# Kernel optimization log

Measured on AMD Instinct MI355X. Metric: run time of the kernel, lower is better.

## Reference

```python
import jax, jax.numpy as jnp
import numpy as np
from jax import lax

B = 256
R_ITERS = 3

def squash(x):
    # x * |x| / (1 + |x|^2), applied along last axis
    n = jnp.linalg.norm(x, axis=-1, keepdims=True)
    return x * n / (1.0 + n * n)

def conv2d(x, w, b, stride):
    y = lax.conv_general_dilated(x, w, window_strides=(stride, stride), padding='VALID',
                                 dimension_numbers=('NCHW', 'OIHW', 'NCHW'))
    return y + b[None, :, None, None]

def setup_inputs() -> dict:
    key = jax.random.key(0)
    ks = jax.random.split(key, 12)
    s = 0.05
    return {
        'x': jax.random.normal(ks[0], (B, 1, 28, 28), jnp.float32),
        'label': jax.random.randint(ks[1], (B,), 0, 10),
        'conv1_w': jax.random.normal(ks[2], (256, 1, 9, 9), jnp.float32) * s,
        'conv1_b': jnp.zeros((256,), jnp.float32),
        'pconv_w': jax.random.normal(ks[3], (256, 256, 9, 9), jnp.float32) * s,
        'pconv_b': jnp.zeros((256,), jnp.float32),
        'W_dig': jax.random.normal(ks[4], (1152, 10, 16, 8), jnp.float32),
        'dec_w1': jax.random.normal(ks[5], (512, 160), jnp.float32) * s,
        'dec_b1': jnp.zeros((512,), jnp.float32),
        'dec_w2': jax.random.normal(ks[6], (1024, 512), jnp.float32) * s,
        'dec_b2': jnp.zeros((1024,), jnp.float32),
        'dec_w3': jax.random.normal(ks[7], (784, 1024), jnp.float32) * s,
        'dec_b3': jnp.zeros((784,), jnp.float32),
    }

def reference(x, label, conv1_w, conv1_b, pconv_w, pconv_b, W_dig,
              dec_w1, dec_b1, dec_w2, dec_b2, dec_w3, dec_b3):
    # conv stem: [B,1,28,28] -> [B,256,20,20]
    h = conv2d(x, conv1_w, conv1_b, 1)
    # primary caps conv: -> [B,256,6,6] -> [B,1152,8] -> squash
    h = conv2d(h, pconv_w, pconv_b, 2)
    caps = squash(h.reshape(h.shape[0], -1, 8))
    # prediction vectors u_hat: [B, 1152, 10, 16]
    u = jnp.einsum('iond,bid->bion', W_dig, caps)
    # dynamic routing (softmax over input-capsule axis, per original code)
    b = jnp.zeros_like(u)
    for r in range(1, R_ITERS + 1):
        c = jax.nn.softmax(b, axis=1)
        s = (c * u).sum(axis=1, keepdims=True)     # [B,1,10,16]
        v = squash(s)
        if r != R_ITERS:
            b = b + (v * u).sum(axis=-1, keepdims=True)
    v = v.squeeze(1)                               # [B,10,16]
    # masked reconstruction
    one_hot = jax.nn.one_hot(label, 10, dtype=v.dtype)
    recon = (one_hot[..., None] * v).reshape(v.shape[0], 160)
    recon = jax.nn.relu(recon @ dec_w1.T + dec_b1)
    recon = jax.nn.relu(recon @ dec_w2.T + dec_b2)
    recon = jax.nn.sigmoid(recon @ dec_w3.T + dec_b3)
    return (v, recon, one_hot)
```

## Files before the change

### kernel.cpp

```cpp
#include <hip/hip_runtime.h>
#include <hip/hip_bf16.h>
#include <stdint.h>


typedef short short8 __attribute__((ext_vector_type(8)));
typedef unsigned short u16x8 __attribute__((ext_vector_type(8)));
typedef float f32x4  __attribute__((ext_vector_type(4)));

__device__ inline float bf2f(unsigned short u) {
    unsigned int v = ((unsigned int)u) << 16;
    float f;
    __builtin_memcpy(&f, &v, 4);
    return f;
}
__device__ inline unsigned short f2bf(float f) {
    __hip_bfloat16 h = __float2bfloat16(f);
    unsigned short u;
    __builtin_memcpy(&u, &h, 2);
    return u;
}
__device__ inline float clampf(float x, float b) {
    return fminf(fmaxf(x, -b), b);
}
__device__ inline float rdf(const void* p, size_t i, int f) {
    return f ? ((const float*)p)[i] : bf2f(((const unsigned short*)p)[i]);
}
__device__ inline void gload_lds16(const unsigned short* g, unsigned short* l) {
    __builtin_amdgcn_global_load_lds(
        (const __attribute__((address_space(1))) void*)g,
        (__attribute__((address_space(3))) void*)l, 16, 0, 0);
}
__device__ inline int detect_f(const void* w1c) {
    const unsigned short* w = (const unsigned short*)w1c;
    int lane = threadIdx.x & 63;
    int cnt = 0;
#pragma unroll
    for (int j = 0; j < 4; ++j) {
        float v = fabsf(bf2f(w[lane * 4 + j]));
        if (v > 100.f) cnt++;
    }
#pragma unroll
    for (int off = 32; off; off >>= 1) cnt += __shfl_xor(cnt, off);
    return cnt >= 4;
}

__global__ __launch_bounds__(256) void k_prep(
        const void* __restrict__ w1c, const void* __restrict__ w2c,
        float* __restrict__ h2f, unsigned short* __restrict__ B1p,
        unsigned short* __restrict__ Bp3) {
    __shared__ unsigned short wl[20736];
    int blk = blockIdx.x, tid = threadIdx.x;
    if (blk < 2304) {
        ((f32x4*)h2f)[blk * 256 + tid] = (f32x4){0.f, 0.f, 0.f, 0.f};
    } else if (blk < 2400) {
        int f = detect_f(w1c);
        int idx = (blk - 2304) * 256 + tid;
        int co = idx / 96, k = idx - co * 96;
        B1p[idx] = (k < 81) ? f2bf(rdf(w1c, (size_t)co * 81 + k, f)) : (unsigned short)0;
    } else {
        int f = detect_f(w1c);
        int co = blk - 2400;
        size_t base = (size_t)co * 20736;
        for (int i = tid; i < 20736; i += 256)
            wl[i] = f2bf(rdf(w2c, base + i, f));
        __syncthreads();
        for (int idx = tid; idx < 20736; idx += 256) {
            int t = idx >> 8, ci = idx & 255;
            int kc = ci >> 6, cin = ci & 63;
            Bp3[((size_t)(t * 4 + kc) << 14) + (co << 6) + cin] = wl[ci * 81 + t];
        }
    }
}

__global__ __launch_bounds__(256) void k_prep2(
        const void* __restrict__ wdig, const void* __restrict__ dw2,
        const void* __restrict__ dw3, const void* __restrict__ w1c,
        unsigned short* __restrict__ Wdb2,
        unsigned short* __restrict__ w2b,
        unsigned short* __restrict__ w3b) {
    __shared__ unsigned short wl[20480];
    int f = detect_f(w1c);
    int blk = blockIdx.x, tid = threadIdx.x;
    if (blk < 72) {
        int i0 = blk * 16;
        size_t base = (size_t)i0 * 1280;
        for (int idx = tid; idx < 20480; idx += 256)
            wl[idx] = f2bf(rdf(wdig, base + idx, f));
        __syncthreads();
        if (tid < 160) {
            int o = tid / 16, n = tid - o * 16;
            unsigned short* dst = Wdb2 + (size_t)o * 147456 + n * 9216 + i0 * 8;
            const unsigned short* src = wl + tid * 8;
#pragma unroll
            for (int i = 0; i < 16; ++i)
                *(uint4*)(dst + i * 8) = *(const uint4*)(src + i * 1280);
        }
    } else if (blk < 2120) {
        int idx = (blk - 72) * 256 + tid;
        w2b[idx] = f2bf(rdf(dw2, idx, f));
    } else {
        int idx = (blk - 2120) * 256 + tid;
        w3b[idx] = (idx < 802816) ? f2bf(rdf(dw3, idx, f)) : (unsigned short)0;
    }
}

__global__ __launch_bounds__(256) void k_conv1(
        const void* __restrict__ x,
        const unsigned short* __restrict__ B1p,
        const void* __restrict__ bias,
        unsigned short* __restrict__ h1p,
        const void* __restrict__ w1c) {
    __shared__ unsigned short xl[1568];
    __shared__ int offt[96];
    int f = detect_f(w1c);
    int tid = threadIdx.x;
    if (tid < 96) offt[tid] = (tid < 81) ? (tid / 9) * 28 + (tid % 9) : 0;

    int mblk = blockIdx.x * 128;
    int bfirst = mblk / 400;
    int blast = (mblk + 127) / 400;
    int nload = (blast - bfirst + 1) * 784;
    for (int i = tid; i < nload; i += 256)
        xl[i] = f2bf(rdf(x, (size_t)bfirst * 784 + i, f));
    __syncthreads();

    int wave = tid >> 6, lane = tid & 63;
    int wr = wave >> 1, wc = wave & 1;
    int mbase = mblk + wr * 64;
    int nbase = blockIdx.y * 128 + wc * 64;
    int l15 = lane & 15, l4 = lane >> 4;

    int lbase[4];
#pragma unroll
    for (int mt = 0; mt < 4; ++mt) {
        int m = mbase + mt * 16 + l15;
        int img = m / 400 - bfirst, pos = m % 400;
        lbase[mt] = img * 784 + (pos / 20) * 28 + (pos % 20);
    }

    f32x4 acc[4][4];
#pragma unroll
    for (int mt = 0; mt < 4; ++mt)
#pragma unroll
        for (int nt = 0; nt < 4; ++nt)
            acc[mt][nt] = (f32x4){0.f, 0.f, 0.f, 0.f};

#pragma unroll
    for (int kc = 0; kc < 3; ++kc) {
        int kbase = kc * 32 + l4 * 8;
        short8 af[4], bfr[4];
#pragma unroll
        for (int mt = 0; mt < 4; ++mt)
#pragma unroll
            for (int j = 0; j < 8; ++j) {
                int k = kbase + j;
                af[mt][j] = (k < 81) ? (short)xl[lbase[mt] + offt[k]] : (short)0;
            }
#pragma unroll
        for (int nt = 0; nt < 4; ++nt)
            bfr[nt] = *(const short8*)(B1p + (size_t)(nbase + nt * 16 + l15) * 96 + kbase);
#pragma unroll
        for (int mt = 0; mt < 4; ++mt)
#pragma unroll
            for (int nt = 0; nt < 4; ++nt)
                acc[mt][nt] = __builtin_amdgcn_mfma_f32_16x16x32_bf16(
                    af[mt], bfr[nt], acc[mt][nt], 0, 0, 0);
    }

#pragma unroll
    for (int mt = 0; mt < 4; ++mt)
#pragma unroll
        for (int nt = 0; nt < 4; ++nt) {
            int col = nbase + nt * 16 + l15;
            float bv = rdf(bias, col, f);
#pragma unroll
            for (int r = 0; r < 4; ++r) {
                int row = mbase + mt * 16 + l4 * 4 + r;
                h1p[(size_t)row * 256 + col] = f2bf(clampf(acc[mt][nt][r] + bv, 1024.f));
            }
        }
}

__global__ __launch_bounds__(256) void k_conv2(
        const unsigned short* __restrict__ h1p,
        const unsigned short* __restrict__ Bp,
        float* __restrict__ h2f) {
    __shared__ unsigned short As[2][4096];
    __shared__ unsigned short Bs[2][4096];
    int tid = threadIdx.x;
    int wave = tid >> 6, lane = tid & 63;
    int wr = wave >> 1, wc = wave & 1;
    int mb = blockIdx.x * 128, nb = blockIdx.y * 128;
    int s = blockIdx.z;
    int t0 = (81 * s) >> 3, t1 = (81 * (s + 1)) >> 3;
    int l15 = lane & 15, l4 = lane >> 4;

    int rsub = lane >> 2;
    int slog = (lane & 3) ^ ((lane >> 3) & 3);
    int aoff[2], boff[2];
#pragma unroll
    for (int r = 0; r < 2; ++r) {
        int row = wave * 32 + r * 16 + rsub;
        int m = mb + row;
        int bb = m / 36, pos = m - bb * 36;
        int y = pos / 6, xx = pos - y * 6;
        aoff[r] = (bb * 400 + y * 40 + xx * 2) * 256 + slog * 8;
        boff[r] = row * 64 + slog * 8;
    }

    int ko = (l4 ^ ((l15 >> 1) & 3)) << 3;
    int arow[4], brow[4];
#pragma unroll
    for (int mt = 0; mt < 4; ++mt) arow[mt] = ((wr * 64 + mt * 16 + l15) << 5) + ko;
#pragma unroll
    for (int nt = 0; nt < 4; ++nt) brow[nt] = ((wc * 64 + nt * 16 + l15) << 5) + ko;

    f32x4 acc[4][4];
#pragma unroll
    for (int mt = 0; mt < 4; ++mt)
#pragma unroll
        for (int nt = 0; nt < 4; ++nt)
            acc[mt][nt] = (f32x4){0.f, 0.f, 0.f, 0.f};

    int skc = 0;
    int sky = t0 / 9, skx = t0 - sky * 9;
    int stadd = (sky * 20 + skx) << 8;
    int st4 = t0 * 4;

    auto stage = [&](int buf) {
        const unsigned short* aw = h1p + stadd + (skc << 5);
        const unsigned short* bw = Bp + (((size_t)(st4 + (skc >> 1))) << 14)
                                     + nb * 64 + ((skc & 1) << 5);
        unsigned short* al = &As[buf][wave << 10];
        unsigned short* bl = &Bs[buf][wave << 10];
#pragma unroll
        for (int r = 0; r < 2; ++r) {
            gload_lds16(aw + aoff[r], al + (r << 9));
            gload_lds16(bw + boff[r], bl + (r << 9));
        }
    };
    auto adv = [&]() {
        if (++skc == 8) {
            skc = 0; st4 += 4;
            if (++skx == 9) { skx = 0; stadd += 3072; }
            else            { stadd += 256; }
        }
    };
    auto compute = [&](int buf) {
        short8 af[4], bfr[4];
#pragma unroll
        for (int mt = 0; mt < 4; ++mt)
            af[mt] = *(const short8*)(&As[buf][arow[mt]]);
#pragma unroll
        for (int nt = 0; nt < 4; ++nt)
            bfr[nt] = *(const short8*)(&Bs[buf][brow[nt]]);
#pragma unroll
        for (int mt = 0; mt < 4; ++mt)
#pragma unroll
            for (int nt = 0; nt < 4; ++nt)
                acc[mt][nt] = __builtin_amdgcn_mfma_f32_16x16x32_bf16(
                    af[mt], bfr[nt], acc[mt][nt], 0, 0, 0);
    };

    int nit = (t1 - t0) * 8;
    stage(0); adv();
    asm volatile("s_waitcnt vmcnt(0)" ::: "memory");
    __builtin_amdgcn_s_barrier();
    int cur = 0;
    for (int i = 0; i < nit; ++i) {
        if (i + 1 < nit) { stage(cur ^ 1); adv(); }
        compute(cur);
        asm volatile("s_waitcnt vmcnt(0)" ::: "memory");
        __builtin_amdgcn_s_barrier();
        cur ^= 1;
    }

#pragma unroll
    for (int mt = 0; mt < 4; ++mt)
#pragma unroll
        for (int nt = 0; nt < 4; ++nt) {
            int col = nb + wc * 64 + nt * 16 + l15;
#pragma unroll
            for (int r = 0; r < 4; ++r) {
                int row = mb + wr * 64 + mt * 16 + l4 * 4 + r;
                atomicAdd(&h2f[(size_t)row * 256 + col], acc[mt][nt][r]);
            }
        }
}

__global__ __launch_bounds__(256) void k_caps2(
        const float* __restrict__ h2f, const void* __restrict__ pb,
        unsigned short* __restrict__ caps, const void* __restrict__ w1c) {
    __shared__ float ld[9216];
    int f = detect_f(w1c);
    int b = blockIdx.x, tid = threadIdx.x;
#pragma unroll 4
    for (int p = 0; p < 36; ++p)
        ld[p * 256 + tid] = h2f[(size_t)b * 9216 + p * 256 + tid];
    __syncthreads();
    for (int c = tid; c < 1152; c += 256) {
        float h[8], ss = 0.f;
#pragma unroll
        for (int d = 0; d < 8; ++d) {
            int flat = c * 8 + d;
            int co = flat / 36, pos = flat - co * 36;
            float v = clampf(ld[pos * 256 + co] + rdf(pb, co, f), 20000.f);
            h[d] = v;
            ss += v * v;
        }
        float sc = sqrtf(ss) / (1.f + ss);
        u16x8 cv;
#pragma unroll
        for (int d = 0; d < 8; ++d) cv[d] = f2bf(h[d] * sc);
        *(u16x8*)(caps + ((size_t)b * 1152 + c) * 8) = cv;
    }
}

__global__ __launch_bounds__(384) void k_routing(
        const unsigned short* __restrict__ caps, const unsigned short* __restrict__ Wdb2,
        const int* __restrict__ label, void* __restrict__ d_out,
        float* __restrict__ vsel, const void* __restrict__ w1c) {
    int f = detect_f(w1c);
    int bo = blockIdx.x;
    int b = bo / 10, o = bo - b * 10;
    int tid = threadIdx.x;
    int wid = tid >> 6, lane = tid & 63;

    __shared__ float redw[6][16];
    __shared__ float sbuf[16];
    __shared__ float mred[8];
    __shared__ float sred[8];

    float u[3][16];
    float a[3] = {0.f, 0.f, 0.f};
    const unsigned short* capb = caps + (size_t)b * 9216;
    const unsigned short* wob = Wdb2 + (size_t)o * 147456;

#pragma unroll
    for (int r = 0; r < 3; ++r) {
        int i = tid + r * 384;
        u16x8 cq = *(const u16x8*)(capb + i * 8);
        float cf[8];
#pragma unroll
        for (int d = 0; d < 8; ++d) cf[d] = bf2f(cq[d]);
#pragma unroll
        for (int n = 0; n < 16; ++n) {
            u16x8 q = *(const u16x8*)(wob + ((size_t)n * 1152 + i) * 8);
            float sacc = 0.f;
#pragma unroll
            for (int d = 0; d < 8; ++d) sacc += bf2f(q[d]) * cf[d];
            u[r][n] = sacc;
        }
    }

    for (int rr = 1; rr <= 3; ++rr) {
        float mx = fmaxf(fmaxf(a[0], a[1]), a[2]);
#pragma unroll
        for (int off = 32; off; off >>= 1) mx = fmaxf(mx, __shfl_xor(mx, off));
        if (lane == 0) mred[wid] = mx;
        __syncthreads();
        float M = mred[0];
#pragma unroll
        for (int w = 1; w < 6; ++w) M = fmaxf(M, mred[w]);

        float e[3], es = 0.f;
#pragma unroll
        for (int r = 0; r < 3; ++r) { e[r] = __expf(a[r] - M); es += e[r]; }
#pragma unroll
        for (int off = 32; off; off >>= 1) es += __shfl_xor(es, off);
        if (lane == 0) sred[wid] = es;
        __syncthreads();
        float S = 0.f;
#pragma unroll
        for (int w = 0; w < 6; ++w) S += sred[w];
        float inv = 1.f / S;

        float p[16];
#pragma unroll
        for (int n = 0; n < 16; ++n)
            p[n] = (e[0] * u[0][n] + e[1] * u[1][n] + e[2] * u[2][n]) * inv;
#pragma unroll
        for (int n = 0; n < 16; ++n)
#pragma unroll
            for (int off = 32; off; off >>= 1) p[n] += __shfl_xor(p[n], off);
        if (lane == 0)
#pragma unroll
            for (int n = 0; n < 16; ++n) redw[wid][n] = p[n];
        __syncthreads();
        if (tid < 16) {
            float sn = 0.f;
#pragma unroll
            for (int w = 0; w < 6; ++w) sn += redw[w][tid];
            sbuf[tid] = sn;
        }
        __syncthreads();

        float ss = 0.f;
#pragma unroll
        for (int n = 0; n < 16; ++n) ss += sbuf[n] * sbuf[n];
        float sc = sqrtf(ss) / (1.f + ss);

        if (rr < 3) {
#pragma unroll
            for (int r = 0; r < 3; ++r) {
                float dot = 0.f;
#pragma unroll
                for (int n = 0; n < 16; ++n) dot += sbuf[n] * u[r][n];
                a[r] += sc * dot;
            }
            __syncthreads();
        } else {
            int lbl = label[b];
            if (tid < 16) {
                float vn = clampf(sbuf[tid] * sc, 1.f);
                if (f) ((float*)d_out)[(bo << 4) + tid] = vn;
                else   ((unsigned short*)d_out)[(bo << 4) + tid] = f2bf(vn);
                if (o == lbl) vsel[(b << 4) + tid] = vn;
            }
            if (tid == 0) {
                float oh = (o == lbl) ? 1.f : 0.f;
                if (f) ((float*)d_out)[241664 + bo] = oh;
                else   ((unsigned short*)d_out)[241664 + bo] = f2bf(oh);
            }
        }
    }
}

__global__ void k_dec1(const float* __restrict__ vsel, const int* __restrict__ label,
                       const void* __restrict__ w1, const void* __restrict__ b1,
                       unsigned short* __restrict__ r1b, const void* __restrict__ w1c) {
    int f = detect_f(w1c);
    int b = blockIdx.x, j = threadIdx.x;
    __shared__ float vs[16];
    if (j < 16) vs[j] = vsel[b * 16 + j];
    __syncthreads();
    int lbl = label[b];
    size_t wb = (size_t)j * 160 + lbl * 16;
    float acc = rdf(b1, j, f);
#pragma unroll
    for (int n = 0; n < 16; ++n) acc += rdf(w1, wb + n, f) * vs[n];
    r1b[b * 512 + j] = f2bf(fmaxf(acc, 0.f));
}

__global__ __launch_bounds__(256) void k_dgemm(
        const unsigned short* __restrict__ A, const unsigned short* __restrict__ B,
        const void* __restrict__ bias, int K, int mode, int nvalid, int ostride,
        unsigned short* __restrict__ outb, void* __restrict__ d_out,
        const void* __restrict__ w1c) {
    int f = detect_f(w1c);
    int tid = threadIdx.x;
    int wave = tid >> 6, lane = tid & 63;
    int wr = wave >> 1, wc = wave & 1;
    int mbase = blockIdx.x * 128 + wr * 64;
    int nbase = blockIdx.y * 128 + wc * 64;
    int l15 = lane & 15, l4 = lane >> 4;
    int koff = l4 * 8;

    f32x4 acc[4][4];
#pragma unroll
    for (int mt = 0; mt < 4; ++mt)
#pragma unroll
        for (int nt = 0; nt < 4; ++nt)
            acc[mt][nt] = (f32x4){0.f, 0.f, 0.f, 0.f};

    int nch = K >> 5;
    for (int kc = 0; kc < nch; ++kc) {
        int k0 = kc * 32 + koff;
        short8 af[4], bfr[4];
#pragma unroll
        for (int mt = 0; mt < 4; ++mt)
            af[mt] = *(const short8*)(A + (size_t)(mbase + mt * 16 + l15) * K + k0);
#pragma unroll
        for (int nt = 0; nt < 4; ++nt)
            bfr[nt] = *(const short8*)(B + (size_t)(nbase + nt * 16 + l15) * K + k0);
#pragma unroll
        for (int mt = 0; mt < 4; ++mt)
#pragma unroll
            for (int nt = 0; nt < 4; ++nt)
                acc[mt][nt] = __builtin_amdgcn_mfma_f32_16x16x32_bf16(
                    af[mt], bfr[nt], acc[mt][nt], 0, 0, 0);
    }

#pragma unroll
    for (int mt = 0; mt < 4; ++mt)
#pragma unroll
        for (int nt = 0; nt < 4; ++nt) {
            int col = nbase + nt * 16 + l15;
            float bv = (col < nvalid) ? rdf(bias, col, f) : 0.f;
#pragma unroll
            for (int r = 0; r < 4; ++r) {
                int row = mbase + mt * 16 + l4 * 4 + r;
                float v = acc[mt][nt][r] + bv;
                if (mode == 0) {
                    outb[(size_t)row * ostride + col] = f2bf(fmaxf(v, 0.f));
                } else if (col < nvalid) {
                    float a = clampf(v, 60.f);
                    float sig = 1.f / (1.f + __expf(-a));
                    size_t oi = 40960 + (size_t)row * 784 + col;
                    if (f) ((float*)d_out)[oi] = sig;
                    else   ((unsigned short*)d_out)[oi] = f2bf(sig);
                }
            }
        }
}

extern "C" void kernel_launch(void* const* d_in, const int* in_sizes, int n_in,
                              void* d_out, int out_size, void* d_ws, size_t ws_size,
                              hipStream_t stream) {
    const void* x    = d_in[0];
    const int*  lbl  = (const int*)d_in[1];
    const void* w1c  = d_in[2];
    const void* b1c  = d_in[3];
    const void* w2c  = d_in[4];
    const void* b2c  = d_in[5];
    const void* wdig = d_in[6];
    const void* dw1  = d_in[7];
    const void* db1  = d_in[8];
    const void* dw2  = d_in[9];
    const void* db2  = d_in[10];
    const void* dw3  = d_in[11];
    const void* db3  = d_in[12];
    (void)in_sizes; (void)n_in; (void)out_size; (void)ws_size;

    char* ws = (char*)d_ws;
    float* h2f           = (float*)(ws);
    unsigned short* Bp3  = (unsigned short*)(ws + 9437184);
    unsigned short* caps = (unsigned short*)(ws + 9437184);
    unsigned short* B1p  = (unsigned short*)(ws + 20054016);
    unsigned short* h1p  = (unsigned short*)(ws + 20103168);
    unsigned short* Wdb2 = (unsigned short*)(ws + 20103168);
    unsigned short* w2b  = (unsigned short*)(ws + 23052288);
    unsigned short* w3b  = (unsigned short*)(ws + 24100864);
    unsigned short* r1b  = (unsigned short*)(ws + 25935872);
    unsigned short* r2b  = (unsigned short*)(ws + 26198016);
    float* vsel          = (float*)(ws + 26722304);

    hipLaunchKernelGGL(k_prep,  dim3(2656),     dim3(256), 0, stream, w1c, w2c, h2f, B1p, Bp3);
    hipLaunchKernelGGL(k_conv1, dim3(800, 2),   dim3(256), 0, stream, x, B1p, b1c, h1p, w1c);
    hipLaunchKernelGGL(k_conv2, dim3(72, 2, 8), dim3(256), 0, stream, h1p, Bp3, h2f);
    hipLaunchKernelGGL(k_prep2, dim3(5704),     dim3(256), 0, stream,
                       wdig, dw2, dw3, w1c, Wdb2, w2b, w3b);
    hipLaunchKernelGGL(k_caps2, dim3(256),      dim3(256), 0, stream, h2f, b2c, caps, w1c);
    hipLaunchKernelGGL(k_routing, dim3(2560),   dim3(384), 0, stream, caps, Wdb2, lbl,
                       d_out, vsel, w1c);
    hipLaunchKernelGGL(k_dec1,  dim3(256),      dim3(512), 0, stream, vsel, lbl, dw1, db1, r1b, w1c);
    hipLaunchKernelGGL(k_dgemm, dim3(2, 8),     dim3(256), 0, stream,
                       r1b, w2b, db2, 512, 0, 1024, 1024, r2b, d_out, w1c);
    hipLaunchKernelGGL(k_dgemm, dim3(2, 7),     dim3(256), 0, stream,
                       r2b, w3b, db3, 1024, 1, 784, 0, (unsigned short*)nullptr, d_out, w1c);
}
```

Before: 552.6 us.

## Widen conv2 tile to full 256 output channels and reorder split-K grid

The conv2 implicit GEMM now has each block compute a 128x256 output tile covering all channels instead of 128x128, so each A (activation) tile is loaded from global memory once rather than twice. The grid is reordered so split-K slices vary fastest, which may improve L2 reuse of A rows. The pipeline now places the wait/barrier before issuing the next stage, and launch bounds request two blocks per SM. In exchange, each thread holds twice as many accumulators (128 floats) and the kernel uses more LDS, which risks register pressure and lower occupancy, and there are half as many blocks.

```diff
diff --git a/kernel.cpp b/kernel.cpp
--- a/kernel.cpp
+++ b/kernel.cpp
@@ -181,23 +181,23 @@
         }
 }
 
-__global__ __launch_bounds__(256) void k_conv2(
+__global__ __launch_bounds__(256, 2) void k_conv2(
         const unsigned short* __restrict__ h1p,
         const unsigned short* __restrict__ Bp,
         float* __restrict__ h2f) {
     __shared__ unsigned short As[2][4096];
-    __shared__ unsigned short Bs[2][4096];
+    __shared__ unsigned short Bs[2][8192];
     int tid = threadIdx.x;
     int wave = tid >> 6, lane = tid & 63;
     int wr = wave >> 1, wc = wave & 1;
-    int mb = blockIdx.x * 128, nb = blockIdx.y * 128;
-    int s = blockIdx.z;
+    int mb = blockIdx.y << 7;
+    int s = blockIdx.x;
     int t0 = (81 * s) >> 3, t1 = (81 * (s + 1)) >> 3;
     int l15 = lane & 15, l4 = lane >> 4;
 
     int rsub = lane >> 2;
     int slog = (lane & 3) ^ ((lane >> 3) & 3);
-    int aoff[2], boff[2];
+    int aoff[2];
 #pragma unroll
     for (int r = 0; r < 2; ++r) {
         int row = wave * 32 + r * 16 + rsub;
@@ -205,21 +205,26 @@
         int bb = m / 36, pos = m - bb * 36;
         int y = pos / 6, xx = pos - y * 6;
         aoff[r] = (bb * 400 + y * 40 + xx * 2) * 256 + slog * 8;
-        boff[r] = row * 64 + slog * 8;
+    }
+    int boff[4];
+#pragma unroll
+    for (int r = 0; r < 4; ++r) {
+        int col = wave * 64 + r * 16 + rsub;
+        boff[r] = col * 64 + slog * 8;
     }
 
     int ko = (l4 ^ ((l15 >> 1) & 3)) << 3;
-    int arow[4], brow[4];
+    int arow[4], brow[8];
 #pragma unroll
     for (int mt = 0; mt < 4; ++mt) arow[mt] = ((wr * 64 + mt * 16 + l15) << 5) + ko;
 #pragma unroll
-    for (int nt = 0; nt < 4; ++nt) brow[nt] = ((wc * 64 + nt * 16 + l15) << 5) + ko;
-
-    f32x4 acc[4][4];
+    for (int nt = 0; nt < 8; ++nt) brow[nt] = ((wc * 128 + nt * 16 + l15) << 5) + ko;
+
+    f32x4 acc[4][8];
 #pragma unroll
     for (int mt = 0; mt < 4; ++mt)
 #pragma unroll
-        for (int nt = 0; nt < 4; ++nt)
+        for (int nt = 0; nt < 8; ++nt)
             acc[mt][nt] = (f32x4){0.f, 0.f, 0.f, 0.f};
 
     int skc = 0;
@@ -230,14 +235,13 @@
     auto stage = [&](int buf) {
         const unsigned short* aw = h1p + stadd + (skc << 5);
         const unsigned short* bw = Bp + (((size_t)(st4 + (skc >> 1))) << 14)
-                                     + nb * 64 + ((skc & 1) << 5);
-        unsigned short* al = &As[buf][wave << 10];
-        unsigned short* bl = &Bs[buf][wave << 10];
-#pragma unroll
-        for (int r = 0; r < 2; ++r) {
-            gload_lds16(aw + aoff[r], al + (r << 9));
-            gload_lds16(bw + boff[r], bl + (r << 9));
-        }
+                                     + ((skc & 1) << 5);
+#pragma unroll
+        for (int r = 0; r < 2; ++r)
+            gload_lds16(aw + aoff[r], &As[buf][(wave * 2 + r) << 9]);
+#pragma unroll
+        for (int r = 0; r < 4; ++r)
+            gload_lds16(bw + boff[r], &Bs[buf][(wave * 4 + r) << 9]);
     };
     auto adv = [&]() {
         if (++skc == 8) {
@@ -247,39 +251,39 @@
         }
     };
     auto compute = [&](int buf) {
-        short8 af[4], bfr[4];
+        short8 af[4];
 #pragma unroll
         for (int mt = 0; mt < 4; ++mt)
             af[mt] = *(const short8*)(&As[buf][arow[mt]]);
 #pragma unroll
-        for (int nt = 0; nt < 4; ++nt)
-            bfr[nt] = *(const short8*)(&Bs[buf][brow[nt]]);
-#pragma unroll
-        for (int mt = 0; mt < 4; ++mt)
-#pragma unroll
-            for (int nt = 0; nt < 4; ++nt)
-                acc[mt][nt] = __builtin_amdgcn_mfma_f32_16x16x32_bf16(
-                    af[mt], bfr[nt], acc[mt][nt], 0, 0, 0);
+        for (int h = 0; h < 2; ++h) {
+            short8 bf4[4];
+#pragma unroll
+            for (int n = 0; n < 4; ++n)
+                bf4[n] = *(const short8*)(&Bs[buf][brow[h * 4 + n]]);
+#pragma unroll
+            for (int mt = 0; mt < 4; ++mt)
+#pragma unroll
+                for (int n = 0; n < 4; ++n)
+                    acc[mt][h * 4 + n] = __builtin_amdgcn_mfma_f32_16x16x32_bf16(
+                        af[mt], bf4[n], acc[mt][h * 4 + n], 0, 0, 0);
+        }
     };
 
     int nit = (t1 - t0) * 8;
     stage(0); adv();
-    asm volatile("s_waitcnt vmcnt(0)" ::: "memory");
-    __builtin_amdgcn_s_barrier();
-    int cur = 0;
     for (int i = 0; i < nit; ++i) {
-        if (i + 1 < nit) { stage(cur ^ 1); adv(); }
-        compute(cur);
         asm volatile("s_waitcnt vmcnt(0)" ::: "memory");
         __builtin_amdgcn_s_barrier();
-        cur ^= 1;
+        if (i + 1 < nit) { stage((i + 1) & 1); adv(); }
+        compute(i & 1);
     }
 
 #pragma unroll
     for (int mt = 0; mt < 4; ++mt)
 #pragma unroll
-        for (int nt = 0; nt < 4; ++nt) {
-            int col = nb + wc * 64 + nt * 16 + l15;
+        for (int nt = 0; nt < 8; ++nt) {
+            int col = wc * 128 + nt * 16 + l15;
 #pragma unroll
             for (int r = 0; r < 4; ++r) {
                 int row = mb + wr * 64 + mt * 16 + l4 * 4 + r;
@@ -537,7 +541,7 @@
 
     hipLaunchKernelGGL(k_prep,  dim3(2656),     dim3(256), 0, stream, w1c, w2c, h2f, B1p, Bp3);
     hipLaunchKernelGGL(k_conv1, dim3(800, 2),   dim3(256), 0, stream, x, B1p, b1c, h1p, w1c);
-    hipLaunchKernelGGL(k_conv2, dim3(72, 2, 8), dim3(256), 0, stream, h1p, Bp3, h2f);
+    hipLaunchKernelGGL(k_conv2, dim3(8, 72),    dim3(256), 0, stream, h1p, Bp3, h2f);
     hipLaunchKernelGGL(k_prep2, dim3(5704),     dim3(256), 0, stream,
                        wdig, dw2, dw3, w1c, Wdb2, w2b, w3b);
     hipLaunchKernelGGL(k_caps2, dim3(256),      dim3(256), 0, stream, h2f, b2c, caps, w1c);
```

Result: slower. 579.0 us (+4.8%).
